# Kernel optimization log

Measured on AMD Instinct MI355X. Metric: run time of the kernel, lower is better.

The kernel has to match this reference:

```python
import jax, jax.numpy as jnp
import numpy as np

B, L, D, H, MAXS = 32, 2048, 1024, 16, 10
DH = D // H

def _ln(x, w, b, eps=1e-5):
    mu = jnp.mean(x, axis=-1, keepdims=True)
    var = jnp.var(x, axis=-1, keepdims=True)
    return (x - mu) * jax.lax.rsqrt(var + eps) * w + b

def setup_inputs() -> dict:
    key = jax.random.key(0)
    ks = jax.random.split(key, 6)
    s = 1.0 / np.sqrt(D)
    return {
        "grid_embeddings": jax.random.normal(ks[0], (B, L, D), dtype=jnp.float32),
        "symbol_queries": jax.random.normal(ks[1], (MAXS, D), dtype=jnp.float32) * 0.02,
        "qn_w": jnp.ones((D,), jnp.float32), "qn_b": jnp.zeros((D,), jnp.float32),
        "in_proj_w": jax.random.uniform(ks[2], (3 * D, D), jnp.float32, -s, s),
        "in_proj_b": jnp.zeros((3 * D,), jnp.float32),
        "out_w": jax.random.uniform(ks[3], (D, D), jnp.float32, -s, s),
        "out_b": jnp.zeros((D,), jnp.float32),
        "on_w": jnp.ones((D,), jnp.float32), "on_b": jnp.zeros((D,), jnp.float32),
        "symbol_position": 3,
    }

def reference(grid_embeddings, symbol_queries, qn_w, qn_b, in_proj_w, in_proj_b,
              out_w, out_b, on_w, on_b, symbol_position):
    Wq, Wk, Wv = in_proj_w[:D], in_proj_w[D:2*D], in_proj_w[2*D:]
    bq, bk, bv = in_proj_b[:D], in_proj_b[D:2*D], in_proj_b[2*D:]
    # query is identical across batch: compute once
    q0 = _ln(symbol_queries[symbol_position], qn_w, qn_b)          # [D]
    q = (q0 @ Wq.T + bq).reshape(H, DH)                             # [H, DH]
    k = (grid_embeddings @ Wk.T + bk).reshape(B, L, H, DH)          # [B, L, H, DH]
    v = (grid_embeddings @ Wv.T + bv).reshape(B, L, H, DH)          # [B, L, H, DH]
    scale = 1.0 / np.sqrt(DH).astype(np.float32)
    scores = jnp.einsum('hd,blhd->bhl', q, k) * scale               # [B, H, L]
    attn = jax.nn.softmax(scores, axis=-1)                          # [B, H, L]
    ctx = jnp.einsum('bhl,blhd->bhd', attn, v).reshape(B, D)        # [B, D]
    pooled = _ln(ctx @ out_w.T + out_b, on_w, on_b)                 # [B, D]
    return pooled, attn[:, :, None, :]                              # [B,H,1,L]
```

## Files before the change

### kernel.cpp

```cpp
#include <hip/hip_runtime.h>
#include <math.h>

#define BB 32
#define LL 2048
#define DD 1024
#define HH 16
#define DHH 64
#define NCK 16
#define CH  128
#define NT  8

#define WS_Q     1024
#define WS_R     2048
#define WS_C     18432
#define WS_CTX   19008
#define WS_Y     51776
#define WS_SSUM  84544
#define WS_PART  92736

#define RED_OFF  65536
#define WT_OFF   69632
#define SMEM_BYTES 71680

typedef __attribute__((ext_vector_type(8))) short    bf16x8;
typedef __attribute__((ext_vector_type(4))) float    f32x4;
typedef __attribute__((ext_vector_type(2))) unsigned u32x2;
typedef __attribute__((ext_vector_type(4))) unsigned short u16x4;

#define MFMA(a, b, c) __builtin_amdgcn_mfma_f32_16x16x32_bf16(a, b, c, 0, 0, 0)

__device__ __forceinline__ unsigned short f2bf(float f) {
    unsigned u = __float_as_uint(f);
    return (unsigned short)((u + 0x7FFFu + ((u >> 16) & 1u)) >> 16);
}
__device__ __forceinline__ float bf2f(unsigned short u) {
    return __uint_as_float((unsigned)u << 16);
}
__device__ __forceinline__ float wave_sum(float v) {
#pragma unroll
    for (int s = 32; s >= 1; s >>= 1) v += __shfl_xor(v, s, 64);
    return v;
}

__global__ void k_q(const float* __restrict__ sq, const float* __restrict__ qn_w,
                    const float* __restrict__ qn_b, const int* __restrict__ pos,
                    const float* __restrict__ ipw, const float* __restrict__ ipb,
                    float* __restrict__ ws) {
    const int t = threadIdx.x;
    const int w = t >> 6, lane = t & 63;
    __shared__ float q0s[DD];
    __shared__ float rs[4], rs2[4];
    {
        const float4 x = ((const float4*)(sq + (size_t)pos[0] * DD))[t];
        float s  = x.x + x.y + x.z + x.w;
        float s2 = x.x * x.x + x.y * x.y + x.z * x.z + x.w * x.w;
        s = wave_sum(s); s2 = wave_sum(s2);
        if (lane == 0) { rs[w] = s; rs2[w] = s2; }
        __syncthreads();
        s  = rs[0] + rs[1] + rs[2] + rs[3];
        s2 = rs2[0] + rs2[1] + rs2[2] + rs2[3];
        const float mu  = s * (1.0f / DD);
        const float var = s2 * (1.0f / DD) - mu * mu;
        const float rstd = rsqrtf(var + 1e-5f);
        const float4 w4 = ((const float4*)qn_w)[t];
        const float4 b4 = ((const float4*)qn_b)[t];
        float4 o;
        o.x = (x.x - mu) * rstd * w4.x + b4.x;
        o.y = (x.y - mu) * rstd * w4.y + b4.y;
        o.z = (x.z - mu) * rstd * w4.z + b4.z;
        o.w = (x.w - mu) * rstd * w4.w + b4.w;
        ((float4*)q0s)[t] = o;
    }
    __syncthreads();
    const int d = blockIdx.x * 4 + w;
    const float* row = ipw + (size_t)d * DD;
    float acc = 0.f;
#pragma unroll
    for (int it = 0; it < 4; ++it) {
        float4 a = ((const float4*)row)[lane + 64 * it];
        float4 b = ((const float4*)q0s)[lane + 64 * it];
        acc += a.x * b.x + a.y * b.y + a.z * b.z + a.w * b.w;
    }
    acc = wave_sum(acc);
    if (lane == 0) (ws + WS_Q)[d] = acc + ipb[d];
}

__global__ void k_r(const float* __restrict__ ipw, const float* __restrict__ ipb,
                    float* __restrict__ ws) {
    const int h = blockIdx.x >> 2, qa = blockIdx.x & 3;
    const int t = threadIdx.x;
    const int e = qa * 256 + t;
    const float* q = ws + WS_Q;
    const float* wk = ipw + (size_t)(DD + h * DHH) * DD;
    float acc = 0.f;
#pragma unroll 8
    for (int j = 0; j < DHH; ++j)
        acc += q[h * DHH + j] * wk[(size_t)j * DD + e];
    (ws + WS_R)[h * DD + e] = acc * 0.125f;
    if (qa == 0 && t < 64) {
        float p = q[h * DHH + t] * ipb[DD + h * DHH + t];
        p = wave_sum(p);
        if (t == 0) (ws + WS_C)[h] = p * 0.125f;
    }
}

__global__ __launch_bounds__(256, 2)
void k_fused(const float* __restrict__ gr, const float* __restrict__ ws,
             float* __restrict__ attn_e, unsigned short* __restrict__ part,
             float* __restrict__ ssum) {
    extern __shared__ char smem[];
    const int b  = blockIdx.x >> 4;
    const int ck = blockIdx.x & 15;
    const int l0 = ck * CH;
    const int t  = threadIdx.x;
    const int wv = t >> 6, lane = t & 63;
    const int c16 = lane & 15, g = lane >> 4;
    const int estrip = wv * 256;

    bf16x8 rpk[8];
#pragma unroll
    for (int ks = 0; ks < 8; ++ks) {
        const float* rp = ws + WS_R + (size_t)c16 * DD + estrip + ks * 32 + g * 8;
        float4 f0 = *(const float4*)rp, f1 = *(const float4*)(rp + 4);
        bf16x8 r;
        r[0] = (short)f2bf(f0.x); r[1] = (short)f2bf(f0.y);
        r[2] = (short)f2bf(f0.z); r[3] = (short)f2bf(f0.w);
        r[4] = (short)f2bf(f1.x); r[5] = (short)f2bf(f1.y);
        r[6] = (short)f2bf(f1.z); r[7] = (short)f2bf(f1.w);
        rpk[ks] = r;
    }
    const float myc = (ws + WS_C)[c16];

    f32x4 pv[16];
#pragma unroll
    for (int i = 0; i < 16; ++i) pv[i] = (f32x4){0.f, 0.f, 0.f, 0.f};
    float s_acc = 0.f;

    const int srow = wv * 4 + ((lane >> 2) & 3);
    const int scol = (lane >> 4) * 16 + (lane & 3) * 4;
    const float* gbase = gr + ((size_t)(b * LL + l0) + srow) * DD + scol;
    const int wr_base = (lane >> 4) * 512 + wv * 128 + ((lane >> 2) & 3) * 32 +
                        (lane & 3) * 8;

    float4 raw[16];
#pragma unroll
    for (int j = 0; j < 16; ++j) raw[j] = *(const float4*)(gbase + 64 * j);
#pragma unroll
    for (int j = 0; j < 16; ++j) {
        u16x4 p = {f2bf(raw[j].x), f2bf(raw[j].y), f2bf(raw[j].z), f2bf(raw[j].w)};
        *(u16x4*)(smem + wr_base + j * 2048) = p;
    }
#pragma unroll
    for (int j = 0; j < 16; ++j)
        raw[j] = *(const float4*)(gbase + 16 * DD + 64 * j);
    __syncthreads();

#pragma unroll 1
    for (int tt = 0; tt < NT; ++tt) {
        const char* rb = smem + (tt & 1) * 32768;
        f32x4 sa = {0.f, 0.f, 0.f, 0.f};
#pragma unroll
        for (int ks = 0; ks < 8; ++ks) {
            const int e16 = wv * 16 + ks * 2 + (g >> 1);
            const int byt = (e16 * 4 + (c16 >> 2)) * 128 + (c16 & 3) * 32 + (g & 1) * 16;
            bf16x8 a = *(const bf16x8*)(rb + byt);
            sa = MFMA(a, rpk[ks], sa);
        }
        *(f32x4*)(smem + RED_OFF + (wv * 64 + lane) * 16) = sa;
        __syncthreads();
        if (tt < NT - 1) {
            char* wb = smem + ((tt + 1) & 1) * 32768;
#pragma unroll
            for (int j = 0; j < 16; ++j) {
                u16x4 p = {f2bf(raw[j].x), f2bf(raw[j].y), f2bf(raw[j].z), f2bf(raw[j].w)};
                *(u16x4*)(wb + wr_base + j * 2048) = p;
            }
            if (tt < NT - 2) {
                const float* gs = gbase + (size_t)(tt + 2) * 16 * DD;
#pragma unroll
                for (int j = 0; j < 16; ++j)
                    raw[j] = *(const float4*)(gs + 64 * j);
            }
        }
        f32x4 tot = {myc, myc, myc, myc};
#pragma unroll
        for (int w2 = 0; w2 < 4; ++w2)
            tot += *(const f32x4*)(smem + RED_OFF + (w2 * 64 + lane) * 16);
        f32x4 ex;
        ex[0] = __expf(tot[0]); ex[1] = __expf(tot[1]);
        ex[2] = __expf(tot[2]); ex[3] = __expf(tot[3]);
        u16x4 wp = {f2bf(ex[0]), f2bf(ex[1]), f2bf(ex[2]), f2bf(ex[3])};
        *(u16x4*)(smem + WT_OFF + wv * 512 + c16 * 32 + g * 8) = wp;
        if (wv == 0) {
            float* ap = attn_e + ((size_t)b * HH + c16) * LL + l0 + tt * 16 + g * 4;
            *(float4*)ap = make_float4(ex[0], ex[1], ex[2], ex[3]);
        }
        s_acc += ex[0] + ex[1] + ex[2] + ex[3];
        bf16x8 afrag;
        if (g < 2) {
            afrag = *(const bf16x8*)(smem + WT_OFF + wv * 512 + c16 * 32 + g * 16);
        } else {
            afrag = (bf16x8){0, 0, 0, 0, 0, 0, 0, 0};
        }
#pragma unroll
        for (int grp = 0; grp < 4; ++grp) {
            u32x2 q[8];
#pragma unroll
            for (int n2 = 0; n2 < 4; ++n2) {
                const int est = wv * 16 + grp * 4 + n2;
                const unsigned ta = (unsigned)((tt & 1) * 32768 + est * 512 +
                                               (g & 1) * 256 + c16 * 8);
                asm volatile("ds_read_b64_tr_b16 %0, %1"
                             : "=v"(q[n2 * 2]) : "v"(ta));
                asm volatile("ds_read_b64_tr_b16 %0, %1 offset:128"
                             : "=v"(q[n2 * 2 + 1]) : "v"(ta));
            }
            asm volatile("s_waitcnt lgkmcnt(0)" ::: "memory");
            __builtin_amdgcn_sched_barrier(0);
#pragma unroll
            for (int n2 = 0; n2 < 4; ++n2) {
                union { unsigned u[4]; bf16x8 v; } bb;
                bb.u[0] = q[n2 * 2][0];     bb.u[1] = q[n2 * 2][1];
                bb.u[2] = q[n2 * 2 + 1][0]; bb.u[3] = q[n2 * 2 + 1][1];
                pv[grp * 4 + n2] = MFMA(afrag, bb.v, pv[grp * 4 + n2]);
            }
        }
        __syncthreads();
    }
    float sv = s_acc;
    sv += __shfl_xor(sv, 16, 64);
    sv += __shfl_xor(sv, 32, 64);
    if (wv == 0 && lane < 16)
        ssum[((size_t)b * NCK + ck) * HH + c16] = sv;
    unsigned short* pp = part + ((size_t)b * NCK + ck) * (HH * DD);
#pragma unroll
    for (int nt = 0; nt < 16; ++nt) {
#pragma unroll
        for (int r2 = 0; r2 < 4; ++r2)
            pp[(size_t)(g * 4 + r2) * DD + estrip + nt * 16 + c16] = f2bf(pv[nt][r2]);
    }
}

__global__ void k_ctx(const float* __restrict__ ipw, const float* __restrict__ ipb,
                      const unsigned short* __restrict__ part,
                      const float* __restrict__ ssum,
                      float* __restrict__ attn_e, float* __restrict__ ctx) {
    const int bh = blockIdx.x, b = bh >> 4, h = bh & 15;
    const int t = threadIdx.x, w = t >> 6, lane = t & 63;
    float S = 0.f;
#pragma unroll
    for (int c = 0; c < NCK; ++c) S += ssum[((size_t)b * NCK + c) * HH + h];
    const float inv = 1.0f / S;
    float4* ar = (float4*)(attn_e + (size_t)bh * LL);
#pragma unroll
    for (int i = 0; i < 2; ++i) {
        float4 v = ar[t + 256 * i];
        v.x *= inv; v.y *= inv; v.z *= inv; v.w *= inv;
        ar[t + 256 * i] = v;
    }
    __shared__ float Xl[DD];
    float4 x = {0.f, 0.f, 0.f, 0.f};
#pragma unroll
    for (int c = 0; c < NCK; ++c) {
        u16x4 p = *(const u16x4*)(part + ((size_t)b * NCK + c) * (HH * DD) +
                                  (size_t)h * DD + t * 4);
        x.x += bf2f(p[0]); x.y += bf2f(p[1]);
        x.z += bf2f(p[2]); x.w += bf2f(p[3]);
    }
    float4 xs = {x.x * inv, x.y * inv, x.z * inv, x.w * inv};
    ((float4*)Xl)[t] = xs;
    __syncthreads();
    for (int jj = 0; jj < 16; ++jj) {
        const int j = w * 16 + jj;
        const float* row = ipw + (size_t)(2 * DD + h * DHH + j) * DD;
        float acc = 0.f;
#pragma unroll
        for (int it = 0; it < 4; ++it) {
            float4 a = ((const float4*)row)[lane + 64 * it];
            float4 p = ((const float4*)Xl)[lane + 64 * it];
            acc += a.x * p.x + a.y * p.y + a.z * p.z + a.w * p.w;
        }
        acc = wave_sum(acc);
        if (lane == 0) ctx[(size_t)b * DD + h * DHH + j] = acc + ipb[2 * DD + h * DHH + j];
    }
}

__global__ void k_y(const float* __restrict__ ow, const float* __restrict__ ob,
                    const float* __restrict__ ctx, float* __restrict__ y) {
    const int blk = blockIdx.x, b = blk >> 4, ch = blk & 15;
    const int t = threadIdx.x, w = t >> 6, lane = t & 63;
    __shared__ float Xl[DD];
    ((float4*)Xl)[t] = ((const float4*)(ctx + (size_t)b * DD))[t];
    __syncthreads();
    for (int jj = 0; jj < 16; ++jj) {
        const int d = ch * 64 + w * 16 + jj;
        const float* row = ow + (size_t)d * DD;
        float acc = 0.f;
#pragma unroll
        for (int it = 0; it < 4; ++it) {
            float4 a = ((const float4*)row)[lane + 64 * it];
            float4 p = ((const float4*)Xl)[lane + 64 * it];
            acc += a.x * p.x + a.y * p.y + a.z * p.z + a.w * p.w;
        }
        acc = wave_sum(acc);
        if (lane == 0) y[(size_t)b * DD + d] = acc + ob[d];
    }
}

__global__ void k_lnout(const float* __restrict__ y, const float* __restrict__ on_w,
                        const float* __restrict__ on_b, float* __restrict__ outp) {
    const int b = blockIdx.x, t = threadIdx.x;
    const float4 x = ((const float4*)(y + (size_t)b * DD))[t];
    float s  = x.x + x.y + x.z + x.w;
    float s2 = x.x * x.x + x.y * x.y + x.z * x.z + x.w * x.w;
    __shared__ float rs[4], rs2[4];
    s = wave_sum(s); s2 = wave_sum(s2);
    const int w = t >> 6, lane = t & 63;
    if (lane == 0) { rs[w] = s; rs2[w] = s2; }
    __syncthreads();
    s  = rs[0] + rs[1] + rs[2] + rs[3];
    s2 = rs2[0] + rs2[1] + rs2[2] + rs2[3];
    const float mu  = s * (1.0f / DD);
    const float var = s2 * (1.0f / DD) - mu * mu;
    const float rstd = rsqrtf(var + 1e-5f);
    const float4 w4 = ((const float4*)on_w)[t];
    const float4 b4 = ((const float4*)on_b)[t];
    float4 o;
    o.x = (x.x - mu) * rstd * w4.x + b4.x;
    o.y = (x.y - mu) * rstd * w4.y + b4.y;
    o.z = (x.z - mu) * rstd * w4.z + b4.z;
    o.w = (x.w - mu) * rstd * w4.w + b4.w;
    ((float4*)(outp + (size_t)b * DD))[t] = o;
}

extern "C" void kernel_launch(void* const* d_in, const int* in_sizes, int n_in,
                              void* d_out, int out_size, void* d_ws, size_t ws_size,
                              hipStream_t stream) {
    const float* gr   = (const float*)d_in[0];
    const float* sq   = (const float*)d_in[1];
    const float* qn_w = (const float*)d_in[2];
    const float* qn_b = (const float*)d_in[3];
    const float* ipw  = (const float*)d_in[4];
    const float* ipb  = (const float*)d_in[5];
    const float* ow   = (const float*)d_in[6];
    const float* ob   = (const float*)d_in[7];
    const float* on_w = (const float*)d_in[8];
    const float* on_b = (const float*)d_in[9];
    const int*   pos  = (const int*)d_in[10];

    float* out  = (float*)d_out;
    float* attn = out + BB * DD;
    float* ws   = (float*)d_ws;
    unsigned short* part16 = (unsigned short*)(ws + WS_PART);

    hipFuncSetAttribute((const void*)k_fused,
                        hipFuncAttributeMaxDynamicSharedMemorySize, SMEM_BYTES);

    k_q<<<256, 256, 0, stream>>>(sq, qn_w, qn_b, pos, ipw, ipb, ws);
    k_r<<<64, 256, 0, stream>>>(ipw, ipb, ws);
    k_fused<<<BB * NCK, 256, SMEM_BYTES, stream>>>(gr, ws, attn,
                                                   part16, ws + WS_SSUM);
    k_ctx<<<BB * HH, 256, 0, stream>>>(ipw, ipb, part16, ws + WS_SSUM,
                                       attn, ws + WS_CTX);
    k_y<<<BB * 16, 256, 0, stream>>>(ow, ob, ws + WS_CTX, ws + WS_Y);
    k_lnout<<<BB, 256, 0, stream>>>(ws + WS_Y, on_w, on_b, out);
}
```

Baseline: 102.9 us.

## Fuse query and key-projection kernels, use packed bf16 conversion, batch LDS reads

Merges the query-projection and key-projection kernels into one launch, where each block recomputes its head's 64 query values in shared memory. This removes a launch and a global round-trip, at the cost of four-fold redundant query work per head. The manual bf16 rounding is replaced with the HIP packed float2-to-bf16 intrinsic so the compiler can emit packed conversion instructions. The transposed LDS reads in the PV stage are batched into 2 groups of 8 instead of 4 groups of 4, which raises register pressure but means fewer waitcnt stalls.

```diff
diff --git a/kernel.cpp b/kernel.cpp
--- a/kernel.cpp
+++ b/kernel.cpp
@@ -1,4 +1,5 @@
 #include <hip/hip_runtime.h>
+#include <hip/hip_bf16.h>
 #include <math.h>
 
 #define BB 32
@@ -10,7 +11,6 @@
 #define CH  128
 #define NT  8
 
-#define WS_Q     1024
 #define WS_R     2048
 #define WS_C     18432
 #define WS_CTX   19008
@@ -29,9 +29,14 @@
 
 #define MFMA(a, b, c) __builtin_amdgcn_mfma_f32_16x16x32_bf16(a, b, c, 0, 0, 0)
 
-__device__ __forceinline__ unsigned short f2bf(float f) {
-    unsigned u = __float_as_uint(f);
-    return (unsigned short)((u + 0x7FFFu + ((u >> 16) & 1u)) >> 16);
+__device__ __forceinline__ ushort2 pk2(float x, float y) {
+    __hip_bfloat162 h = __float22bfloat162_rn(make_float2(x, y));
+    return *reinterpret_cast<ushort2*>(&h);
+}
+__device__ __forceinline__ u16x4 pk4(float4 f) {
+    ushort2 a = pk2(f.x, f.y), b = pk2(f.z, f.w);
+    u16x4 r; r[0] = a.x; r[1] = a.y; r[2] = b.x; r[3] = b.y;
+    return r;
 }
 __device__ __forceinline__ float bf2f(unsigned short u) {
     return __uint_as_float((unsigned)u << 16);
@@ -42,13 +47,14 @@
     return v;
 }
 
-__global__ void k_q(const float* __restrict__ sq, const float* __restrict__ qn_w,
-                    const float* __restrict__ qn_b, const int* __restrict__ pos,
-                    const float* __restrict__ ipw, const float* __restrict__ ipb,
-                    float* __restrict__ ws) {
-    const int t = threadIdx.x;
-    const int w = t >> 6, lane = t & 63;
+__global__ void k_qr(const float* __restrict__ sq, const float* __restrict__ qn_w,
+                     const float* __restrict__ qn_b, const int* __restrict__ pos,
+                     const float* __restrict__ ipw, const float* __restrict__ ipb,
+                     float* __restrict__ ws) {
+    const int h = blockIdx.x >> 2, qa = blockIdx.x & 3;
+    const int t = threadIdx.x, w = t >> 6, lane = t & 63;
     __shared__ float q0s[DD];
+    __shared__ float qs[DHH];
     __shared__ float rs[4], rs2[4];
     {
         const float4 x = ((const float4*)(sq + (size_t)pos[0] * DD))[t];
@@ -72,33 +78,29 @@
         ((float4*)q0s)[t] = o;
     }
     __syncthreads();
-    const int d = blockIdx.x * 4 + w;
-    const float* row = ipw + (size_t)d * DD;
-    float acc = 0.f;
-#pragma unroll
-    for (int it = 0; it < 4; ++it) {
-        float4 a = ((const float4*)row)[lane + 64 * it];
-        float4 b = ((const float4*)q0s)[lane + 64 * it];
-        acc += a.x * b.x + a.y * b.y + a.z * b.z + a.w * b.w;
-    }
-    acc = wave_sum(acc);
-    if (lane == 0) (ws + WS_Q)[d] = acc + ipb[d];
-}
-
-__global__ void k_r(const float* __restrict__ ipw, const float* __restrict__ ipb,
-                    float* __restrict__ ws) {
-    const int h = blockIdx.x >> 2, qa = blockIdx.x & 3;
-    const int t = threadIdx.x;
+    for (int jj = 0; jj < 16; ++jj) {
+        const int j = w * 16 + jj;
+        const float* row = ipw + (size_t)(h * DHH + j) * DD;
+        float acc = 0.f;
+#pragma unroll
+        for (int it = 0; it < 4; ++it) {
+            float4 a = ((const float4*)row)[lane + 64 * it];
+            float4 b = ((const float4*)q0s)[lane + 64 * it];
+            acc += a.x * b.x + a.y * b.y + a.z * b.z + a.w * b.w;
+        }
+        acc = wave_sum(acc);
+        if (lane == 0) qs[j] = acc + ipb[h * DHH + j];
+    }
+    __syncthreads();
     const int e = qa * 256 + t;
-    const float* q = ws + WS_Q;
     const float* wk = ipw + (size_t)(DD + h * DHH) * DD;
     float acc = 0.f;
 #pragma unroll 8
     for (int j = 0; j < DHH; ++j)
-        acc += q[h * DHH + j] * wk[(size_t)j * DD + e];
+        acc += qs[j] * wk[(size_t)j * DD + e];
     (ws + WS_R)[h * DD + e] = acc * 0.125f;
     if (qa == 0 && t < 64) {
-        float p = q[h * DHH + t] * ipb[DD + h * DHH + t];
+        float p = qs[t] * ipb[DD + h * DHH + t];
         p = wave_sum(p);
         if (t == 0) (ws + WS_C)[h] = p * 0.125f;
     }
@@ -121,12 +123,11 @@
 #pragma unroll
     for (int ks = 0; ks < 8; ++ks) {
         const float* rp = ws + WS_R + (size_t)c16 * DD + estrip + ks * 32 + g * 8;
-        float4 f0 = *(const float4*)rp, f1 = *(const float4*)(rp + 4);
+        u16x4 lo = pk4(*(const float4*)rp);
+        u16x4 hi = pk4(*(const float4*)(rp + 4));
         bf16x8 r;
-        r[0] = (short)f2bf(f0.x); r[1] = (short)f2bf(f0.y);
-        r[2] = (short)f2bf(f0.z); r[3] = (short)f2bf(f0.w);
-        r[4] = (short)f2bf(f1.x); r[5] = (short)f2bf(f1.y);
-        r[6] = (short)f2bf(f1.z); r[7] = (short)f2bf(f1.w);
+        r[0] = (short)lo[0]; r[1] = (short)lo[1]; r[2] = (short)lo[2]; r[3] = (short)lo[3];
+        r[4] = (short)hi[0]; r[5] = (short)hi[1]; r[6] = (short)hi[2]; r[7] = (short)hi[3];
         rpk[ks] = r;
     }
     const float myc = (ws + WS_C)[c16];
@@ -146,10 +147,8 @@
 #pragma unroll
     for (int j = 0; j < 16; ++j) raw[j] = *(const float4*)(gbase + 64 * j);
 #pragma unroll
-    for (int j = 0; j < 16; ++j) {
-        u16x4 p = {f2bf(raw[j].x), f2bf(raw[j].y), f2bf(raw[j].z), f2bf(raw[j].w)};
-        *(u16x4*)(smem + wr_base + j * 2048) = p;
-    }
+    for (int j = 0; j < 16; ++j)
+        *(u16x4*)(smem + wr_base + j * 2048) = pk4(raw[j]);
 #pragma unroll
     for (int j = 0; j < 16; ++j)
         raw[j] = *(const float4*)(gbase + 16 * DD + 64 * j);
@@ -171,10 +170,8 @@
         if (tt < NT - 1) {
             char* wb = smem + ((tt + 1) & 1) * 32768;
 #pragma unroll
-            for (int j = 0; j < 16; ++j) {
-                u16x4 p = {f2bf(raw[j].x), f2bf(raw[j].y), f2bf(raw[j].z), f2bf(raw[j].w)};
-                *(u16x4*)(wb + wr_base + j * 2048) = p;
-            }
+            for (int j = 0; j < 16; ++j)
+                *(u16x4*)(wb + wr_base + j * 2048) = pk4(raw[j]);
             if (tt < NT - 2) {
                 const float* gs = gbase + (size_t)(tt + 2) * 16 * DD;
 #pragma unroll
@@ -189,7 +186,7 @@
         f32x4 ex;
         ex[0] = __expf(tot[0]); ex[1] = __expf(tot[1]);
         ex[2] = __expf(tot[2]); ex[3] = __expf(tot[3]);
-        u16x4 wp = {f2bf(ex[0]), f2bf(ex[1]), f2bf(ex[2]), f2bf(ex[3])};
+        u16x4 wp = pk4(make_float4(ex[0], ex[1], ex[2], ex[3]));
         *(u16x4*)(smem + WT_OFF + wv * 512 + c16 * 32 + g * 8) = wp;
         if (wv == 0) {
             float* ap = attn_e + ((size_t)b * HH + c16) * LL + l0 + tt * 16 + g * 4;
@@ -203,11 +200,11 @@
             afrag = (bf16x8){0, 0, 0, 0, 0, 0, 0, 0};
         }
 #pragma unroll
-        for (int grp = 0; grp < 4; ++grp) {
-            u32x2 q[8];
-#pragma unroll
-            for (int n2 = 0; n2 < 4; ++n2) {
-                const int est = wv * 16 + grp * 4 + n2;
+        for (int pp2 = 0; pp2 < 2; ++pp2) {
+            u32x2 q[16];
+#pragma unroll
+            for (int n2 = 0; n2 < 8; ++n2) {
+                const int est = wv * 16 + pp2 * 8 + n2;
                 const unsigned ta = (unsigned)((tt & 1) * 32768 + est * 512 +
                                                (g & 1) * 256 + c16 * 8);
                 asm volatile("ds_read_b64_tr_b16 %0, %1"
@@ -218,11 +215,11 @@
             asm volatile("s_waitcnt lgkmcnt(0)" ::: "memory");
             __builtin_amdgcn_sched_barrier(0);
 #pragma unroll
-            for (int n2 = 0; n2 < 4; ++n2) {
+            for (int n2 = 0; n2 < 8; ++n2) {
                 union { unsigned u[4]; bf16x8 v; } bb;
                 bb.u[0] = q[n2 * 2][0];     bb.u[1] = q[n2 * 2][1];
                 bb.u[2] = q[n2 * 2 + 1][0]; bb.u[3] = q[n2 * 2 + 1][1];
-                pv[grp * 4 + n2] = MFMA(afrag, bb.v, pv[grp * 4 + n2]);
+                pv[pp2 * 8 + n2] = MFMA(afrag, bb.v, pv[pp2 * 8 + n2]);
             }
         }
         __syncthreads();
@@ -236,8 +233,10 @@
 #pragma unroll
     for (int nt = 0; nt < 16; ++nt) {
 #pragma unroll
-        for (int r2 = 0; r2 < 4; ++r2)
-            pp[(size_t)(g * 4 + r2) * DD + estrip + nt * 16 + c16] = f2bf(pv[nt][r2]);
+        for (int r2 = 0; r2 < 4; ++r2) {
+            ushort2 u = pk2(pv[nt][r2], pv[nt][r2]);
+            pp[(size_t)(g * 4 + r2) * DD + estrip + nt * 16 + c16] = u.x;
+        }
     }
 }
 
@@ -356,8 +355,7 @@
     hipFuncSetAttribute((const void*)k_fused,
                         hipFuncAttributeMaxDynamicSharedMemorySize, SMEM_BYTES);
 
-    k_q<<<256, 256, 0, stream>>>(sq, qn_w, qn_b, pos, ipw, ipb, ws);
-    k_r<<<64, 256, 0, stream>>>(ipw, ipb, ws);
+    k_qr<<<64, 256, 0, stream>>>(sq, qn_w, qn_b, pos, ipw, ipb, ws);
     k_fused<<<BB * NCK, 256, SMEM_BYTES, stream>>>(gr, ws, attn,
                                                    part16, ws + WS_SSUM);
     k_ctx<<<BB * HH, 256, 0, stream>>>(ipw, ipb, part16, ws + WS_SSUM,
```

Result: slower. 108.3 us (+5.3%).

## Split fused attention block across 8 waves instead of 4

Applied to the files above, without the earlier changes.

Doubles the k_fused block to 512 threads, so each wave owns a 128-element strip of D instead of 256. Per-thread score fragments, PV accumulators and staged load registers are halved, and the cross-wave score reduction now sums 8 partials. The shared reduction buffer grows and the attention-row store rotates across waves. This is meant to add latency hiding and memory-level parallelism for the HBM-bound stream, at the cost of more cross-wave reduction traffic and a larger shared-memory footprint per block.

```diff
diff --git a/kernel.cpp b/kernel.cpp
--- a/kernel.cpp
+++ b/kernel.cpp
@@ -19,8 +19,8 @@
 #define WS_PART  92736
 
 #define RED_OFF  65536
-#define WT_OFF   69632
-#define SMEM_BYTES 71680
+#define WT_OFF   73728
+#define SMEM_BYTES 77824
 
 typedef __attribute__((ext_vector_type(8))) short    bf16x8;
 typedef __attribute__((ext_vector_type(4))) float    f32x4;
@@ -32,6 +32,10 @@
 __device__ __forceinline__ unsigned short f2bf(float f) {
     unsigned u = __float_as_uint(f);
     return (unsigned short)((u + 0x7FFFu + ((u >> 16) & 1u)) >> 16);
+}
+__device__ __forceinline__ u16x4 pk4(float4 f) {
+    u16x4 r; r[0] = f2bf(f.x); r[1] = f2bf(f.y); r[2] = f2bf(f.z); r[3] = f2bf(f.w);
+    return r;
 }
 __device__ __forceinline__ float bf2f(unsigned short u) {
     return __uint_as_float((unsigned)u << 16);
@@ -104,7 +108,7 @@
     }
 }
 
-__global__ __launch_bounds__(256, 2)
+__global__ __launch_bounds__(512, 2)
 void k_fused(const float* __restrict__ gr, const float* __restrict__ ws,
              float* __restrict__ attn_e, unsigned short* __restrict__ part,
              float* __restrict__ ssum) {
@@ -115,11 +119,11 @@
     const int t  = threadIdx.x;
     const int wv = t >> 6, lane = t & 63;
     const int c16 = lane & 15, g = lane >> 4;
-    const int estrip = wv * 256;
-
-    bf16x8 rpk[8];
-#pragma unroll
-    for (int ks = 0; ks < 8; ++ks) {
+    const int estrip = wv * 128;
+
+    bf16x8 rpk[4];
+#pragma unroll
+    for (int ks = 0; ks < 4; ++ks) {
         const float* rp = ws + WS_R + (size_t)c16 * DD + estrip + ks * 32 + g * 8;
         float4 f0 = *(const float4*)rp, f1 = *(const float4*)(rp + 4);
         bf16x8 r;
@@ -131,28 +135,26 @@
     }
     const float myc = (ws + WS_C)[c16];
 
-    f32x4 pv[16];
-#pragma unroll
-    for (int i = 0; i < 16; ++i) pv[i] = (f32x4){0.f, 0.f, 0.f, 0.f};
+    f32x4 pv[8];
+#pragma unroll
+    for (int i = 0; i < 8; ++i) pv[i] = (f32x4){0.f, 0.f, 0.f, 0.f};
     float s_acc = 0.f;
 
-    const int srow = wv * 4 + ((lane >> 2) & 3);
-    const int scol = (lane >> 4) * 16 + (lane & 3) * 4;
-    const float* gbase = gr + ((size_t)(b * LL + l0) + srow) * DD + scol;
-    const int wr_base = (lane >> 4) * 512 + wv * 128 + ((lane >> 2) & 3) * 32 +
-                        (lane & 3) * 8;
-
-    float4 raw[16];
-#pragma unroll
-    for (int j = 0; j < 16; ++j) raw[j] = *(const float4*)(gbase + 64 * j);
-#pragma unroll
-    for (int j = 0; j < 16; ++j) {
-        u16x4 p = {f2bf(raw[j].x), f2bf(raw[j].y), f2bf(raw[j].z), f2bf(raw[j].w)};
-        *(u16x4*)(smem + wr_base + j * 2048) = p;
-    }
-#pragma unroll
-    for (int j = 0; j < 16; ++j)
-        raw[j] = *(const float4*)(gbase + 16 * DD + 64 * j);
+    const int srow = ((lane >> 2) & 3) + (wv & 3) * 4;
+    const int se0  = (lane & 3) * 4 + ((lane >> 4) + (wv >> 2) * 4) * 16;
+    const float* gbase = gr + ((size_t)(b * LL + l0) + srow) * DD + se0;
+    const int wr_base = ((lane >> 4) + (wv >> 2) * 4) * 512 + (wv & 3) * 128 +
+                        ((lane >> 2) & 3) * 32 + (lane & 3) * 8;
+
+    float4 raw[8];
+#pragma unroll
+    for (int j = 0; j < 8; ++j) raw[j] = *(const float4*)(gbase + 128 * j);
+#pragma unroll
+    for (int j = 0; j < 8; ++j)
+        *(u16x4*)(smem + wr_base + j * 4096) = pk4(raw[j]);
+#pragma unroll
+    for (int j = 0; j < 8; ++j)
+        raw[j] = *(const float4*)(gbase + 16 * DD + 128 * j);
     __syncthreads();
 
 #pragma unroll 1
@@ -160,8 +162,8 @@
         const char* rb = smem + (tt & 1) * 32768;
         f32x4 sa = {0.f, 0.f, 0.f, 0.f};
 #pragma unroll
-        for (int ks = 0; ks < 8; ++ks) {
-            const int e16 = wv * 16 + ks * 2 + (g >> 1);
+        for (int ks = 0; ks < 4; ++ks) {
+            const int e16 = wv * 8 + ks * 2 + (g >> 1);
             const int byt = (e16 * 4 + (c16 >> 2)) * 128 + (c16 & 3) * 32 + (g & 1) * 16;
             bf16x8 a = *(const bf16x8*)(rb + byt);
             sa = MFMA(a, rpk[ks], sa);
@@ -171,27 +173,25 @@
         if (tt < NT - 1) {
             char* wb = smem + ((tt + 1) & 1) * 32768;
 #pragma unroll
-            for (int j = 0; j < 16; ++j) {
-                u16x4 p = {f2bf(raw[j].x), f2bf(raw[j].y), f2bf(raw[j].z), f2bf(raw[j].w)};
-                *(u16x4*)(wb + wr_base + j * 2048) = p;
-            }
+            for (int j = 0; j < 8; ++j)
+                *(u16x4*)(wb + wr_base + j * 4096) = pk4(raw[j]);
             if (tt < NT - 2) {
                 const float* gs = gbase + (size_t)(tt + 2) * 16 * DD;
 #pragma unroll
-                for (int j = 0; j < 16; ++j)
-                    raw[j] = *(const float4*)(gs + 64 * j);
+                for (int j = 0; j < 8; ++j)
+                    raw[j] = *(const float4*)(gs + 128 * j);
             }
         }
         f32x4 tot = {myc, myc, myc, myc};
 #pragma unroll
-        for (int w2 = 0; w2 < 4; ++w2)
+        for (int w2 = 0; w2 < 8; ++w2)
             tot += *(const f32x4*)(smem + RED_OFF + (w2 * 64 + lane) * 16);
         f32x4 ex;
         ex[0] = __expf(tot[0]); ex[1] = __expf(tot[1]);
         ex[2] = __expf(tot[2]); ex[3] = __expf(tot[3]);
-        u16x4 wp = {f2bf(ex[0]), f2bf(ex[1]), f2bf(ex[2]), f2bf(ex[3])};
-        *(u16x4*)(smem + WT_OFF + wv * 512 + c16 * 32 + g * 8) = wp;
-        if (wv == 0) {
+        *(u16x4*)(smem + WT_OFF + wv * 512 + c16 * 32 + g * 8) =
+            pk4(make_float4(ex[0], ex[1], ex[2], ex[3]));
+        if (wv == (tt & 7)) {
             float* ap = attn_e + ((size_t)b * HH + c16) * LL + l0 + tt * 16 + g * 4;
             *(float4*)ap = make_float4(ex[0], ex[1], ex[2], ex[3]);
         }
@@ -203,11 +203,11 @@
             afrag = (bf16x8){0, 0, 0, 0, 0, 0, 0, 0};
         }
 #pragma unroll
-        for (int grp = 0; grp < 4; ++grp) {
+        for (int grp = 0; grp < 2; ++grp) {
             u32x2 q[8];
 #pragma unroll
             for (int n2 = 0; n2 < 4; ++n2) {
-                const int est = wv * 16 + grp * 4 + n2;
+                const int est = wv * 8 + grp * 4 + n2;
                 const unsigned ta = (unsigned)((tt & 1) * 32768 + est * 512 +
                                                (g & 1) * 256 + c16 * 8);
                 asm volatile("ds_read_b64_tr_b16 %0, %1"
@@ -234,7 +234,7 @@
         ssum[((size_t)b * NCK + ck) * HH + c16] = sv;
     unsigned short* pp = part + ((size_t)b * NCK + ck) * (HH * DD);
 #pragma unroll
-    for (int nt = 0; nt < 16; ++nt) {
+    for (int nt = 0; nt < 8; ++nt) {
 #pragma unroll
         for (int r2 = 0; r2 < 4; ++r2)
             pp[(size_t)(g * 4 + r2) * DD + estrip + nt * 16 + c16] = f2bf(pv[nt][r2]);
@@ -358,7 +358,7 @@
 
     k_q<<<256, 256, 0, stream>>>(sq, qn_w, qn_b, pos, ipw, ipb, ws);
     k_r<<<64, 256, 0, stream>>>(ipw, ipb, ws);
-    k_fused<<<BB * NCK, 256, SMEM_BYTES, stream>>>(gr, ws, attn,
+    k_fused<<<BB * NCK, 512, SMEM_BYTES, stream>>>(gr, ws, attn,
                                                    part16, ws + WS_SSUM);
     k_ctx<<<BB * HH, 256, 0, stream>>>(ipw, ipb, part16, ws + WS_SSUM,
                                        attn, ws + WS_CTX);
```

After: 103.8 us. No clear change (+0.9%).
